# Kernel tuning notes

Hardware: AMD Instinct MI355X
Metric: run time of the kernel (lower is better)

Reference implementation:

```python
import jax, jax.numpy as jnp
import numpy as np

RESO = 32
SPLIT = 4
HEADS = 16  # block-level heads; each branch uses HEADS//2
DIM = 512
MLP_HID = 2048
EPS = 1e-5


def layer_norm(x, g, b):
    m = jnp.mean(x, axis=-1, keepdims=True)
    v = jnp.mean(jnp.square(x - m), axis=-1, keepdims=True)
    return (x - m) * jax.lax.rsqrt(v + EPS) * g + b


def dwconv3x3(x, w, b):
    # x: [N, C, Hs, Ws], w: [C, 1, 3, 3] (torch depthwise layout), b: [C]
    y = jax.lax.conv_general_dilated(
        x, w, window_strides=(1, 1), padding='SAME',
        feature_group_count=x.shape[1],
        dimension_numbers=('NCHW', 'OIHW', 'NCHW'))
    return y + b[None, :, None, None]


def cswin_branch(q, k, v, reso, Hs, Ws, heads, lepe_w, lepe_b):
    # q,k,v: [B, L, C] with L = reso^3; attention windows are Hs*Ws tokens,
    # window batch = B * D * (H/Hs) * (W/Ws) (depth folded into batch).
    B, L, C = q.shape
    hd = C // heads
    D = H = W = reso
    scale = hd ** -0.5

    def to_win(t):  # [B,L,C] -> [Bw, heads, Hs*Ws, hd]
        t = t.transpose(0, 2, 1).reshape(B, C, D, H // Hs, Hs, W // Ws, Ws)
        t = t.transpose(0, 2, 3, 5, 4, 6, 1).reshape(-1, Hs * Ws, heads, hd)
        return t.transpose(0, 2, 1, 3)

    qh = to_win(q)
    kh = to_win(k)
    # v windows kept in [Bw, C, Hs, Ws] image layout for the LePE depthwise conv
    vw = v.transpose(0, 2, 1).reshape(B, C, D, H // Hs, Hs, W // Ws, Ws)
    vw = vw.transpose(0, 2, 3, 5, 1, 4, 6).reshape(-1, C, Hs, Ws)
    lepe = dwconv3x3(vw, lepe_w, lepe_b)
    lepe = lepe.reshape(-1, heads, hd, Hs * Ws).transpose(0, 1, 3, 2)
    vh = vw.reshape(-1, heads, hd, Hs * Ws).transpose(0, 1, 3, 2)

    attn = jax.nn.softmax((qh * scale) @ jnp.swapaxes(kh, -1, -2), axis=-1)
    o = attn @ vh + lepe  # [Bw, heads, Hs*Ws, hd]

    # windows2img back to [B, L, C]
    o = o.transpose(0, 2, 1, 3).reshape(-1, Hs * Ws, C)
    o = o.reshape(B, D, H // Hs, W // Ws, Hs, Ws, C)
    o = o.transpose(0, 1, 2, 4, 3, 5, 6).reshape(B, D * H * W, C)
    return o


def setup_inputs() -> dict:
    key = jax.random.key(0)
    ks = jax.random.split(key, 16)
    C, Cb, hid = DIM, DIM // 2, MLP_HID

    def lin(k, fan_in, shape):
        return (jax.random.normal(k, shape, jnp.float32) * (fan_in ** -0.5))

    return {
        'x': jax.random.normal(ks[0], (1, C, RESO, RESO, RESO), jnp.float32),
        'norm1_g': jnp.ones((C,), jnp.float32),
        'norm1_b': jnp.zeros((C,), jnp.float32),
        'qkv_w': lin(ks[1], C, (C, 3 * C)),
        'lepe0_w': lin(ks[2], 9, (Cb, 1, 3, 3)),
        'lepe0_b': jnp.zeros((Cb,), jnp.float32),
        'lepe1_w': lin(ks[3], 9, (Cb, 1, 3, 3)),
        'lepe1_b': jnp.zeros((Cb,), jnp.float32),
        'proj_w': lin(ks[4], C, (C, C)),
        'proj_b': jnp.zeros((C,), jnp.float32),
        'norm2_g': jnp.ones((C,), jnp.float32),
        'norm2_b': jnp.zeros((C,), jnp.float32),
        'fc1_w': lin(ks[5], C, (C, hid)),
        'fc1_b': jnp.zeros((hid,), jnp.float32),
        'fc2_w': lin(ks[6], hid, (hid, C)),
        'fc2_b': jnp.zeros((C,), jnp.float32),
    }


def reference(x, norm1_g, norm1_b, qkv_w, lepe0_w, lepe0_b, lepe1_w, lepe1_b,
              proj_w, proj_b, norm2_g, norm2_b, fc1_w, fc1_b, fc2_w, fc2_b):
    B, C = x.shape[0], x.shape[1]
    reso = x.shape[2]
    xc = jnp.transpose(x, (0, 2, 3, 4, 1))  # [B,D,H,W,C]
    img = layer_norm(xc, norm1_g, norm1_b)
    qkv = jnp.einsum('bdhwc,co->bdhwo', img, qkv_w).reshape(B, -1, 3, C)
    q, k, v = qkv[:, :, 0], qkv[:, :, 1], qkv[:, :, 2]

    Ch = C // 2
    hh = HEADS // 2
    # branch 0: idx=0 -> H_sp=reso, W_sp=split ; branch 1: idx=1 -> H_sp=split, W_sp=reso
    x1 = cswin_branch(q[..., :Ch], k[..., :Ch], v[..., :Ch], reso, reso, SPLIT, hh, lepe0_w, lepe0_b)
    x2 = cswin_branch(q[..., Ch:], k[..., Ch:], v[..., Ch:], reso, SPLIT, reso, hh, lepe1_w, lepe1_b)
    att = jnp.concatenate([x1, x2], axis=2) @ proj_w + proj_b

    xf = xc.reshape(B, -1, C) + att
    h = layer_norm(xf, norm2_g, norm2_b)
    h = jax.nn.gelu(h @ fc1_w + fc1_b, approximate=False) @ fc2_w + fc2_b
    xf = xf + h
    out = xf.reshape(B, reso, reso, reso, C).transpose(0, 4, 1, 2, 3)
    return out
```

## Files before the change

### kernel.cpp

```cpp
#include <hip/hip_runtime.h>
#include <hip/hip_bf16.h>
#include <stdint.h>

typedef uint16_t u16;
typedef __attribute__((ext_vector_type(8))) short short8;
typedef __attribute__((ext_vector_type(4))) float floatx4;

#define MFMA(a, b, c) __builtin_amdgcn_mfma_f32_16x16x32_bf16((a), (b), (c), 0, 0, 0)
#define AS1(p) ((const __attribute__((address_space(1))) void*)(p))
#define AS3(p) ((__attribute__((address_space(3))) void*)(p))

static __device__ __forceinline__ float u2f(u16 u) {
    return __uint_as_float(((uint32_t)u) << 16);
}
static __device__ __forceinline__ u16 f2u(float f) {
    union { __hip_bfloat16 h; u16 u; } cv;
    cv.h = __float2bfloat16(f);
    return cv.u;
}
static __device__ __forceinline__ float ldf(const void* p, size_t i, bool f32m) {
    return f32m ? ((const float*)p)[i] : u2f(((const u16*)p)[i]);
}
static __device__ __forceinline__ short8 ld8(const void* p, size_t i, bool f32m) {
    if (f32m) {
        const float* f = (const float*)p + i;
        short8 o;
#pragma unroll
        for (int j = 0; j < 8; ++j) o[j] = (short)f2u(f[j]);
        return o;
    }
    return *reinterpret_cast<const short8*>((const u16*)p + i);
}
static __device__ __forceinline__ void st8(void* p, size_t i, const float* v, bool f32m) {
    if (f32m) {
        float* f = (float*)p + i;
#pragma unroll
        for (int j = 0; j < 8; ++j) f[j] = v[j];
    } else {
        short8 o;
#pragma unroll
        for (int j = 0; j < 8; ++j) o[j] = (short)f2u(v[j]);
        *reinterpret_cast<short8*>((u16*)p + i) = o;
    }
}
static __device__ __forceinline__ float gelu_f(float u) {
    float y = 1.5957691216057308f * (u + 0.044715f * u * u * u);
    return u / (1.f + __expf(-y));
}
static __device__ __forceinline__ void pl32swap(uint32_t& a, uint32_t& b) {
    asm volatile("v_permlane32_swap_b32 %0, %1" : "+v"(a), "+v"(b));
}

__global__ __launch_bounds__(256) void detect_dtype(const u16* __restrict__ x,
                                                    int* __restrict__ flag)
{
    const int tid = threadIdx.x;
    int cnt = 0;
    for (int i = tid; i < 4096; i += 256) {
        int e = (x[i] >> 7) & 0xFF;
        if (e >= 0xBE) ++cnt;
    }
#pragma unroll
    for (int m = 32; m >= 1; m >>= 1) cnt += __shfl_xor(cnt, m);
    __shared__ int s[4];
    if ((tid & 63) == 0) s[tid >> 6] = cnt;
    __syncthreads();
    if (tid == 0) flag[0] = (s[0] + s[1] + s[2] + s[3] >= 64) ? 1 : 0;
}

template <int MODE>
__global__ __launch_bounds__(256) void transpose_k(
    const void* __restrict__ src, void* __restrict__ dst, long dstOff,
    int R, int Cc, int dstS,
    const u16* __restrict__ add,
    const int* __restrict__ dflag, int srcSel, int dstSel)
{
    const bool iF = dflag[0] != 0;
    const bool sF = srcSel && iF;
    const bool dF = dstSel && iF;
    __shared__ __align__(16) u16 tile[64][72];
    const int tid = threadIdx.x;
    const int r0 = blockIdx.y * 64;
    const int c0 = blockIdx.x * 64;
#pragma unroll
    for (int s = 0; s < 2; ++s) {
        int ch = tid + s * 256;
        int ir = ch >> 3, ic = (ch & 7) * 8;
        short8 v = ld8(src, (size_t)(r0 + ir) * Cc + c0 + ic, sF);
        if constexpr (MODE == 3) {
            short8 a = *reinterpret_cast<const short8*>(add + (size_t)(r0 + ir) * Cc + c0 + ic);
#pragma unroll
            for (int j = 0; j < 8; ++j)
                tile[ir][ic + j] = f2u(u2f((u16)v[j]) + u2f((u16)a[j]));
        } else {
#pragma unroll
            for (int j = 0; j < 8; ++j) tile[ir][ic + j] = (u16)v[j];
        }
    }
    __syncthreads();
#pragma unroll
    for (int s = 0; s < 2; ++s) {
        int ch = tid + s * 256;
        int jr = ch >> 3, jc = (ch & 7) * 8;
        float f[8];
#pragma unroll
        for (int j = 0; j < 8; ++j) f[j] = u2f(tile[jc + j][jr]);
        st8(dst, (size_t)dstOff + (size_t)(c0 + jr) * dstS + r0 + jc, f, dF);
    }
}

__global__ __launch_bounds__(256) void tln64(
    const void* __restrict__ x, const void* __restrict__ g, const void* __restrict__ b,
    u16* __restrict__ O, u16* __restrict__ XT, const int* __restrict__ dflag)
{
    const bool iF = dflag[0] != 0;
    __shared__ __align__(16) u16 tile[64][520];
    const int tid = threadIdx.x;
    const int lane = tid & 63, w = tid >> 6;
    const int t0 = blockIdx.x * 64;
    for (int ct = 0; ct < 8; ++ct) {
#pragma unroll
        for (int s = 0; s < 2; ++s) {
            const int ch = tid + s * 256;
            const int ir = ch >> 3;
            const int ic = (ch & 7) * 8;
            const int c = ct * 64 + ir;
            short8 v = ld8(x, (size_t)c * 32768 + t0 + ic, iF);
            const int c8 = c >> 3;
            const int cl = c & 7;
#pragma unroll
            for (int j = 0; j < 8; ++j) {
                const int t = ic + j;
                const int pg = c8 ^ ((t >> 3) & 3);
                tile[t][pg * 8 + cl] = (u16)v[j];
            }
        }
    }
    __syncthreads();
    float gv[8], bv[8];
#pragma unroll
    for (int jj = 0; jj < 8; ++jj) {
        gv[jj] = ldf(g, lane * 8 + jj, iF);
        bv[jj] = ldf(b, lane * 8 + jj, iF);
    }
    for (int tt = 0; tt < 16; ++tt) {
        const int t = w * 16 + tt;
        const int pg = lane ^ ((t >> 3) & 3);
        short8 v = *reinterpret_cast<const short8*>(&tile[t][pg * 8]);
        *reinterpret_cast<short8*>(XT + (size_t)(t0 + t) * 512 + lane * 8) = v;
        float f[8];
        float s = 0.f, sq = 0.f;
#pragma unroll
        for (int jj = 0; jj < 8; ++jj) { f[jj] = u2f((u16)v[jj]); s += f[jj]; sq += f[jj] * f[jj]; }
#pragma unroll
        for (int m = 32; m >= 1; m >>= 1) { s += __shfl_xor(s, m); sq += __shfl_xor(sq, m); }
        const float mean = s * (1.f / 512.f);
        const float var = sq * (1.f / 512.f) - mean * mean;
        const float rstd = rsqrtf(var + 1e-5f);
        short8 o;
#pragma unroll
        for (int jj = 0; jj < 8; ++jj)
            o[jj] = (short)f2u((f[jj] - mean) * rstd * gv[jj] + bv[jj]);
        *reinterpret_cast<short8*>(O + (size_t)(t0 + t) * 512 + lane * 8) = o;
    }
}

__global__ __launch_bounds__(256) void ln512(
    const u16* __restrict__ X, const void* __restrict__ g, const void* __restrict__ b,
    u16* __restrict__ O, const int* __restrict__ dflag)
{
    const bool iF = dflag[0] != 0;
    const int wid = threadIdx.x >> 6, lane = threadIdx.x & 63;
    const int row = blockIdx.x * 4 + wid;
    const size_t base = (size_t)row * 512 + lane * 8;
    short8 v = *reinterpret_cast<const short8*>(X + base);
    float f[8];
    float s = 0.f, sq = 0.f;
#pragma unroll
    for (int j = 0; j < 8; ++j) { f[j] = u2f((u16)v[j]); s += f[j]; sq += f[j] * f[j]; }
#pragma unroll
    for (int m = 32; m >= 1; m >>= 1) { s += __shfl_xor(s, m); sq += __shfl_xor(sq, m); }
    const float mean = s * (1.f / 512.f);
    const float var = sq * (1.f / 512.f) - mean * mean;
    const float rstd = rsqrtf(var + 1e-5f);
    short8 o;
#pragma unroll
    for (int j = 0; j < 8; ++j)
        o[j] = (short)f2u((f[j] - mean) * rstd * ldf(g, lane * 8 + j, iF)
                          + ldf(b, lane * 8 + j, iF));
    *reinterpret_cast<short8*>(O + base) = o;
}

template <int EPI>
__global__ __launch_bounds__(256) void gemm_bt(
    const u16* __restrict__ A, const u16* __restrict__ Bt,
    const void* __restrict__ bias,
    u16* __restrict__ Cout, int Nt, int N, int K, const int* __restrict__ dflag)
{
    const bool iF = dflag[0] != 0;
    __shared__ __align__(16) u16 As[2][128 * 32];
    __shared__ __align__(16) u16 Bs[2][128 * 32];
    const int bidf = blockIdx.x;
    const int xcd = bidf & 7;
    const int j = bidf >> 3;
    const int m_blk = (j / Nt) * 8 + xcd;
    const int n_blk = j % Nt;
    const int tid = threadIdx.x;
    const int lane = tid & 63, wid = tid >> 6;
    const int wm = wid >> 1, wn = wid & 1;
    const int quad = lane >> 4, l15 = lane & 15;

    floatx4 zero4 = {0.f, 0.f, 0.f, 0.f};
    floatx4 acc[4][4];
#pragma unroll
    for (int i = 0; i < 4; ++i)
#pragma unroll
        for (int jj = 0; jj < 4; ++jj) acc[i][jj] = zero4;

    const u16* Ab = A + (size_t)m_blk * 128 * K;
    const u16* Bb = Bt + (size_t)n_blk * 128 * K;
    const int r0 = tid >> 2;
    const int k0o = (tid & 3) * 8;

    for (int kk = 0; kk < K; kk += 64) {
        if (kk) __syncthreads();
#pragma unroll
        for (int h = 0; h < 2; ++h) {
            const int kg = kk + h * 32 + k0o;
            char* dA = (char*)As[h] + wid * 1024;
            char* dB = (char*)Bs[h] + wid * 1024;
            __builtin_amdgcn_global_load_lds(AS1(Ab + (size_t)r0 * K + kg),        AS3(dA), 16, 0, 0);
            __builtin_amdgcn_global_load_lds(AS1(Ab + (size_t)(r0 + 64) * K + kg), AS3(dA + 4096), 16, 0, 0);
            __builtin_amdgcn_global_load_lds(AS1(Bb + (size_t)r0 * K + kg),        AS3(dB), 16, 0, 0);
            __builtin_amdgcn_global_load_lds(AS1(Bb + (size_t)(r0 + 64) * K + kg), AS3(dB + 4096), 16, 0, 0);
        }
        __syncthreads();
#pragma unroll
        for (int h = 0; h < 2; ++h) {
            short8 af[4], bfv[4];
#pragma unroll
            for (int i = 0; i < 4; ++i)
                af[i] = *reinterpret_cast<const short8*>(&As[h][(wm * 64 + i * 16 + l15) * 32 + quad * 8]);
#pragma unroll
            for (int jj = 0; jj < 4; ++jj)
                bfv[jj] = *reinterpret_cast<const short8*>(&Bs[h][(wn * 64 + jj * 16 + l15) * 32 + quad * 8]);
#pragma unroll
            for (int i = 0; i < 4; ++i)
#pragma unroll
                for (int jj = 0; jj < 4; ++jj)
                    acc[i][jj] = MFMA(af[i], bfv[jj], acc[i][jj]);
        }
    }

    const int m_base = m_blk * 128 + wm * 64 + quad * 4;
    const int n_base = n_blk * 128 + wn * 64 + l15;
#pragma unroll
    for (int i = 0; i < 4; ++i) {
#pragma unroll
        for (int jj = 0; jj < 4; ++jj) {
            const int n = n_base + jj * 16;
            float badd = 0.f;
            if constexpr (EPI >= 1) badd = ldf(bias, n, iF);
#pragma unroll
            for (int r = 0; r < 4; ++r) {
                const int m = m_base + i * 16 + r;
                float v = acc[i][jj][r] + badd;
                if constexpr (EPI == 3) v = gelu_f(v);
                Cout[(size_t)m * N + n] = f2u(v);
            }
        }
    }
}

#define STG(slot, mat, kh, Gb, kcol) do {                                        \
    char* _d = (char*)&L[(slot)][(mat)][(kh)][0] + ldsofs;                       \
    __builtin_amdgcn_global_load_lds(AS1((Gb) + (size_t)srow0 * K + (kcol) + scol0),         AS3(_d),        16, 0, 0); \
    __builtin_amdgcn_global_load_lds(AS1((Gb) + (size_t)(srow0 + 128) * K + (kcol) + scol0), AS3(_d + 8192), 16, 0, 0); \
} while (0)

#define VMW(n) do { asm volatile("s_waitcnt vmcnt(" #n ")" ::: "memory");        \
                    __builtin_amdgcn_sched_barrier(0); } while (0)

#define PHASE(s, kh, nq, STAGE_STMT, WAIT_STMT) do {                             \
    const char* Au = (const char*)&L[(s)][0][(kh)][0];                           \
    const char* Bu = (const char*)&L[(s)][1][(kh)][0];                           \
    if ((nq) == 0) {                                                             \
        _Pragma("unroll")                                                        \
        for (int mf = 0; mf < 8; ++mf)                                           \
            af[mf] = *reinterpret_cast<const short8*>(Au + aoff[mf]);            \
    }                                                                            \
    short8 b0 = *reinterpret_cast<const short8*>(Bu + boff[nq][0]);              \
    short8 b1 = *reinterpret_cast<const short8*>(Bu + boff[nq][1]);              \
    STAGE_STMT;                                                                  \
    asm volatile("s_barrier" ::: "memory");                                      \
    asm volatile("s_waitcnt lgkmcnt(0)" ::: "memory");                           \
    __builtin_amdgcn_sched_barrier(0);                                           \
    __builtin_amdgcn_s_setprio(1);                                               \
    _Pragma("unroll")                                                            \
    for (int mf = 0; mf < 8; ++mf) {                                             \
        acc[mf][(nq) * 2]     = MFMA(af[mf], b0, acc[mf][(nq) * 2]);             \
        acc[mf][(nq) * 2 + 1] = MFMA(af[mf], b1, acc[mf][(nq) * 2 + 1]);         \
    }                                                                            \
    __builtin_amdgcn_s_setprio(0);                                               \
    WAIT_STMT;                                                                   \
    asm volatile("s_barrier" ::: "memory");                                      \
} while (0)

#define GROUP(g, W2, W4, S12, S34) do {                                          \
    const int _s = (g) & 1;                                                      \
    PHASE(_s, 0, 0, if (S12) STG(_s ^ 1, 0, 1, Ab, ((g) + 1) * 64 + 32), (void)0); \
    PHASE(_s, 0, 1, if (S12) STG(_s ^ 1, 1, 1, Bb, ((g) + 1) * 64 + 32), W2);    \
    PHASE(_s, 1, 0, if (S34) STG(_s,     0, 0, Ab, ((g) + 2) * 64),      (void)0); \
    PHASE(_s, 1, 1, if (S34) STG(_s,     1, 0, Bb, ((g) + 2) * 64),      W4);    \
} while (0)

template <int EPI>
__global__ __launch_bounds__(512, 2) void gemm256_bt(
    const u16* __restrict__ A, const u16* __restrict__ Bt,
    const void* __restrict__ bias,
    u16* __restrict__ Cout, int Nt, int N, int K,
    const u16* __restrict__ xadd,
    const int* __restrict__ dflag)
{
    const bool iF = dflag[0] != 0;
    __shared__ __align__(16) u16 L[2][2][2][8192];
    const int bidf = blockIdx.x;
    const int xcd = bidf & 7;
    const int j = bidf >> 3;
    const int m_blk = (j / Nt) * 8 + xcd;
    const int n_blk = j % Nt;
    const int tid = threadIdx.x;
    const int lane = tid & 63, wid = tid >> 6;
    const int wm = wid >> 2, wn = wid & 3;
    const int quad = lane >> 4, l15 = lane & 15;

    const int srow0 = wid * 16 + (lane >> 2);
    const int scol0 = ((lane & 3) ^ ((srow0 >> 1) & 3)) * 8;
    const int ldsofs = wid * 1024;

    const u16* Ab = A + (size_t)m_blk * 256 * K;
    const u16* Bb = Bt + (size_t)n_blk * 256 * K;

    const int sq = (quad ^ ((l15 >> 1) & 3)) << 4;
    int aoff[8], boff[2][2];
#pragma unroll
    for (int mf = 0; mf < 8; ++mf)
        aoff[mf] = (wm * 128 + mf * 16 + l15) * 64 + sq;
#pragma unroll
    for (int nq = 0; nq < 2; ++nq)
#pragma unroll
        for (int jj = 0; jj < 2; ++jj)
            boff[nq][jj] = (wn * 64 + nq * 32 + jj * 16 + l15) * 64 + sq;

    floatx4 zero4 = {0.f, 0.f, 0.f, 0.f};
    floatx4 acc[8][4];
#pragma unroll
    for (int i = 0; i < 8; ++i)
#pragma unroll
        for (int jj = 0; jj < 4; ++jj) acc[i][jj] = zero4;
    short8 af[8];

    const int NG = K >> 6;

    STG(0, 0, 0, Ab, 0);
    STG(0, 1, 0, Bb, 0);
    STG(0, 0, 1, Ab, 32);
    STG(0, 1, 1, Bb, 32);
    STG(1, 0, 0, Ab, 64);
    STG(1, 1, 0, Bb, 64);
    VMW(8);
    asm volatile("s_barrier" ::: "memory");

    int g = 0;
    for (; g < NG - 2; ++g) GROUP(g, VMW(8), VMW(8), true, true);
    GROUP(g, VMW(8), VMW(4), true, false); ++g;
    GROUP(g, VMW(0), (void)0, false, false);

    const int m0 = m_blk * 256 + wm * 128 + quad * 4;
    const int n0 = n_blk * 256 + wn * 64 + l15;
#pragma unroll
    for (int mf = 0; mf < 8; ++mf) {
#pragma unroll
        for (int nf = 0; nf < 4; ++nf) {
            const int n = n0 + nf * 16;
            float badd = 0.f;
            if constexpr (EPI >= 1) badd = ldf(bias, n, iF);
#pragma unroll
            for (int r = 0; r < 4; ++r) {
                const int m = m0 + mf * 16 + r;
                float v = acc[mf][nf][r] + badd;
                if constexpr (EPI == 2) v += u2f(xadd[(size_t)m * 512 + n]);
                if constexpr (EPI == 3) v = gelu_f(v);
                Cout[(size_t)m * N + n] = f2u(v);
            }
        }
    }
}

__global__ __launch_bounds__(256) void cswin_attn(
    const u16* __restrict__ qkv,
    const void* __restrict__ lepe0_w, const void* __restrict__ lepe0_b,
    const void* __restrict__ lepe1_w, const void* __restrict__ lepe1_b,
    u16* __restrict__ att, const int* __restrict__ dflag)
{
    const bool iF = dflag[0] != 0;
    __shared__ __align__(16) u16 q_s[4096];
    __shared__ __align__(16) u16 k_s[4096];
    __shared__ __align__(16) u16 vt_s[32 * 130];
    __shared__ float lw_s[32 * 9];
    __shared__ float lb_s[32];

    const int bid = blockIdx.x;
    const int branch = bid >> 11;
    const int rr = bid & 2047;
    const int win = rr >> 3, head = rr & 7;
    const int d = win >> 3, blk = win & 7;
    const int tid = threadIdx.x;
    const int lane = tid & 63, wid = tid >> 6;
    const int quad = lane >> 4, l15 = lane & 15;
    const int choff = branch * 256 + head * 32;
    const int dbase = d * 1024;

    const void* lw = branch ? lepe1_w : lepe0_w;
    const void* lbp = branch ? lepe1_b : lepe0_b;
    for (int i = tid; i < 288; i += 256) lw_s[i] = ldf(lw, head * 288 + i, iF);
    if (tid < 32) lb_s[tid] = ldf(lbp, head * 32 + tid, iF);

#pragma unroll
    for (int s = 0; s < 2; ++s) {
        int ch = tid + s * 256;
        int t = ch >> 2, e0 = (ch & 3) * 8;
        int l = branch ? (dbase + blk * 128 + t)
                       : (dbase + (t >> 2) * 32 + blk * 4 + (t & 3));
        size_t rowo = (size_t)l * 1536 + choff + e0;
        short8 qv = *reinterpret_cast<const short8*>(qkv + rowo);
        short8 kv = *reinterpret_cast<const short8*>(qkv + rowo + 512);
        short8 vv = *reinterpret_cast<const short8*>(qkv + rowo + 1024);
        const int sw = ((ch >> 3) & 3) << 3;
        *reinterpret_cast<short8*>(&q_s[(ch * 8) ^ sw]) = qv;
        *reinterpret_cast<short8*>(&k_s[(ch * 8) ^ sw]) = kv;
#pragma unroll
        for (int j = 0; j < 8; ++j) vt_s[(e0 + j) * 130 + t] = (u16)vv[j];
    }
    __syncthreads();

    floatx4 zero4 = {0.f, 0.f, 0.f, 0.f};
    const int sq8 = (quad ^ ((l15 >> 1) & 3)) * 8;
    short8 qf[2];
#pragma unroll
    for (int qi = 0; qi < 2; ++qi)
        qf[qi] = *reinterpret_cast<const short8*>(&q_s[(wid * 32 + qi * 16 + l15) * 32 + sq8]);
    floatx4 st[8][2];
#pragma unroll
    for (int kt = 0; kt < 8; ++kt) { st[kt][0] = zero4; st[kt][1] = zero4; }
#pragma unroll
    for (int kt = 0; kt < 8; ++kt) {
        short8 kf = *reinterpret_cast<const short8*>(&k_s[(kt * 16 + l15) * 32 + sq8]);
        st[kt][0] = MFMA(kf, qf[0], st[kt][0]);
        st[kt][1] = MFMA(kf, qf[1], st[kt][1]);
    }

    const float scale = 0.17677669529663687f;
    float inv[2];
#pragma unroll
    for (int qi = 0; qi < 2; ++qi) {
        float sum = 0.f;
#pragma unroll
        for (int kt = 0; kt < 8; ++kt)
#pragma unroll
            for (int r = 0; r < 4; ++r) {
                float v = __expf(st[kt][qi][r] * scale);
                st[kt][qi][r] = v;
                sum += v;
            }
        sum += __shfl_xor(sum, 16);
        sum += __shfl_xor(sum, 32);
        inv[qi] = 1.f / sum;
    }
    uint32_t pk[2][8][2];
#pragma unroll
    for (int qi = 0; qi < 2; ++qi)
#pragma unroll
        for (int kt = 0; kt < 8; ++kt)
#pragma unroll
            for (int u = 0; u < 2; ++u)
                pk[qi][kt][u] = (uint32_t)f2u(st[kt][qi][2 * u] * inv[qi])
                              | ((uint32_t)f2u(st[kt][qi][2 * u + 1] * inv[qi]) << 16);
#pragma unroll
    for (int qi = 0; qi < 2; ++qi)
#pragma unroll
        for (int t = 0; t < 4; ++t)
#pragma unroll
            for (int u = 0; u < 2; ++u)
                pl32swap(pk[qi][2 * t][u], pk[qi][2 * t + 1][u]);

    const uint32_t* v32 = (const uint32_t*)vt_s;
    const int hi4 = (lane >> 4) & 1;
    floatx4 oacc[2][2];
#pragma unroll
    for (int qi = 0; qi < 2; ++qi) { oacc[qi][0] = zero4; oacc[qi][1] = zero4; }
#pragma unroll
    for (int ks = 0; ks < 4; ++ks) {
        const int kq = ks * 16 + quad * 4;
        union { uint32_t w[4]; short8 s; } bv[2];
#pragma unroll
        for (int j = 0; j < 2; ++j) {
            const int chan = j * 16 + l15;
#pragma unroll
            for (int q = 0; q < 4; ++q) bv[j].w[q] = v32[chan * 65 + kq + q];
        }
#pragma unroll
        for (int qi = 0; qi < 2; ++qi) {
            const uint32_t a0 = pk[qi][2 * ks][0],     a1 = pk[qi][2 * ks][1];
            const uint32_t b0 = pk[qi][2 * ks + 1][0], b1 = pk[qi][2 * ks + 1][1];
            const uint32_t s0 = (uint32_t)__shfl_xor((int)a0, 16);
            const uint32_t s1 = (uint32_t)__shfl_xor((int)a1, 16);
            const uint32_t t0 = (uint32_t)__shfl_xor((int)b0, 16);
            const uint32_t t1 = (uint32_t)__shfl_xor((int)b1, 16);
            union { uint32_t w[4]; short8 s; } gw;
            gw.w[0] = hi4 ? t0 : a0;
            gw.w[1] = hi4 ? t1 : a1;
            gw.w[2] = hi4 ? b0 : s0;
            gw.w[3] = hi4 ? b1 : s1;
            oacc[qi][0] = MFMA(gw.s, bv[0].s, oacc[qi][0]);
            oacc[qi][1] = MFMA(gw.s, bv[1].s, oacc[qi][1]);
        }
    }

    const int Hs = branch ? 4 : 32;
    const int Wsz = branch ? 32 : 4;
    const int wsl = branch ? 5 : 2;
    const int wmask = Wsz - 1;
#pragma unroll
    for (int ii = 0; ii < 2; ++ii) {
        const int t0 = wid * 32 + ii * 16 + quad * 4;
        const int hi0 = t0 >> wsl;
        const int w0 = t0 & wmask;
        const int y0 = (hi0 > 0) ? -1 : 0;
        const int y1 = (hi0 < Hs - 1) ? 1 : 0;
        const bool xm = (w0 > 0);
        const bool xp = (w0 + 4 < Wsz);
#pragma unroll
        for (int j = 0; j < 2; ++j) {
            const int e = j * 16 + l15;
            float val[4];
#pragma unroll
            for (int r = 0; r < 4; ++r) val[r] = oacc[ii][j][r] + lb_s[e];
            const uint32_t* vrow = v32 + e * 65;
            const float* wrow = &lw_s[e * 9];
            for (int dy = y0; dy <= y1; ++dy) {
                const int rowb = (hi0 + dy) << wsl;
                const int wlo = rowb >> 1;
                const int whi = wlo + (Wsz >> 1) - 1;
                const int wb = wlo + (w0 >> 1);
                int c0 = wb - 1; if (c0 < wlo) c0 = wlo;
                int c3 = wb + 2; if (c3 > whi) c3 = whi;
                const uint32_t u0 = vrow[c0];
                const uint32_t u1 = vrow[wb];
                const uint32_t u2 = vrow[wb + 1];
                const uint32_t u3 = vrow[c3];
                const float em1 = __uint_as_float(u0 & 0xffff0000u);
                const float f0 = __uint_as_float(u1 << 16);
                const float f1 = __uint_as_float(u1 & 0xffff0000u);
                const float f2 = __uint_as_float(u2 << 16);
                const float f3 = __uint_as_float(u2 & 0xffff0000u);
                const float f4 = __uint_as_float(u3 << 16);
                const float* w3 = wrow + (dy + 1) * 3;
                const float wl = w3[0], wc = w3[1], wp = w3[2];
                const float wl0 = xm ? wl : 0.f;
                const float wp3 = xp ? wp : 0.f;
                val[0] += wl0 * em1 + wc * f0 + wp * f1;
                val[1] += wl * f0 + wc * f1 + wp * f2;
                val[2] += wl * f1 + wc * f2 + wp * f3;
                val[3] += wl * f2 + wc * f3 + wp3 * f4;
            }
#pragma unroll
            for (int r = 0; r < 4; ++r) {
                const int t = t0 + r;
                const int l = branch ? (dbase + blk * 128 + t)
                                     : (dbase + (t >> 2) * 32 + blk * 4 + (t & 3));
                att[(size_t)l * 512 + choff + e] = f2u(val[r]);
            }
        }
    }
}

extern "C" void kernel_launch(void* const* d_in, const int* in_sizes, int n_in,
                              void* d_out, int out_size, void* d_ws, size_t ws_size,
                              hipStream_t stream)
{
    const void* x      = d_in[0];
    const void* n1g    = d_in[1];
    const void* n1b    = d_in[2];
    const void* qkv_w  = d_in[3];
    const void* l0w    = d_in[4];
    const void* l0b    = d_in[5];
    const void* l1w    = d_in[6];
    const void* l1b    = d_in[7];
    const void* proj_w = d_in[8];
    const void* proj_b = d_in[9];
    const void* n2g    = d_in[10];
    const void* n2b    = d_in[11];
    const void* fc1_w  = d_in[12];
    const void* fc1_b  = d_in[13];
    const void* fc2_w  = d_in[14];
    const void* fc2_b  = d_in[15];

    const size_t MB = 1ull << 20;
    if (ws_size < 104 * MB) return;

    char* w = (char*)d_ws;
    u16* qkvT  = (u16*)(w + 0 * MB);
    u16* projT = (u16*)(w + 2 * MB);
    u16* fc1T  = (u16*)(w + 3 * MB);
    u16* fc2T  = (u16*)(w + 5 * MB);
    int* flag  = (int*)(w + 7 * MB);
    u16* qkvb  = (u16*)(w + 8 * MB);
    u16* xf    = (u16*)(w + 40 * MB);
    u16* ln2oc = (u16*)(w + 8 * MB);
    u16* yf    = (u16*)(w + 72 * MB);
    u16* img   = (u16*)d_out;
    u16* xT    = (u16*)d_out + 16777216;
    u16* attb  = (u16*)d_out;
    u16* h1c   = (u16*)d_out;

    const dim3 B(256);
    const dim3 B512(512);
    const u16* NUL = nullptr;
    const void* NULV = nullptr;

    detect_dtype<<<dim3(1), B, 0, stream>>>((const u16*)x, flag);

    transpose_k<0><<<dim3(24, 8), B, 0, stream>>>(qkv_w, qkvT, 0, 512, 1536, 512, NUL, flag, 1, 0);
    transpose_k<0><<<dim3(8, 8),  B, 0, stream>>>(proj_w, projT, 0, 512, 512, 512, NUL, flag, 1, 0);
    transpose_k<0><<<dim3(32, 8), B, 0, stream>>>(fc1_w, fc1T, 0, 512, 2048, 512, NUL, flag, 1, 0);
    transpose_k<0><<<dim3(8, 32), B, 0, stream>>>(fc2_w, fc2T, 0, 2048, 512, 2048, NUL, flag, 1, 0);

    tln64<<<dim3(512), B, 0, stream>>>(x, n1g, n1b, img, xT, flag);

    gemm256_bt<0><<<dim3(128 * 6), B512, 0, stream>>>(img, qkvT, NULV, qkvb, 6, 1536, 512, NUL, flag);

    cswin_attn<<<dim3(4096), B, 0, stream>>>(qkvb, l0w, l0b, l1w, l1b, attb, flag);

    gemm256_bt<2><<<dim3(128 * 2), B512, 0, stream>>>(attb, projT, proj_b, xf, 2, 512, 512, xT, flag);

    for (int i = 0; i < 2; ++i) {
        const size_t off = (size_t)i * 16384 * 512;
        ln512<<<dim3(4096), B, 0, stream>>>(xf + off, n2g, n2b, ln2oc, flag);
        gemm256_bt<3><<<dim3(64 * 8), B512, 0, stream>>>(ln2oc, fc1T, fc1_b, h1c, 8, 2048, 512, NUL, flag);
        gemm_bt<1><<<dim3(128 * 4), B, 0, stream>>>(h1c, fc2T, fc2_b, yf + off, 4, 512, 2048, flag);
    }
    transpose_k<3><<<dim3(8, 512), B, 0, stream>>>(yf, d_out, 0, 32768, 512, 32768, xf, flag, 0, 1);
}
```

Before: 603.9 us.

## Fold LayerNorm2 into fc1 GEMM epilogue and fuse residual transpose into fc2

Replaces the per-chunk LayerNorm kernel with a single row-stats pass and folds the norm algebraically into the fc1 GEMM: gamma is pre-multiplied into the transposed fc1 weights, and the epilogue applies mean/rstd plus the precomputed column sums of gamma*W and beta*W. The fc2 GEMM epilogue now adds the residual and writes directly in transposed NCDHW layout, removing the final transpose kernel and the yf buffer. The fc1 output is split across two workspace buffers. The aim is to remove a full read/write pass of the normalized activations and the final transpose, at the cost of uncoalesced 4-element transposed stores and some precision change from the folded norm.

Measured after the change: 633.0 us. 1.05x slower.

```diff
diff --git a/kernel.cpp b/kernel.cpp
--- a/kernel.cpp
+++ b/kernel.cpp
@@ -87,15 +87,8 @@
         int ch = tid + s * 256;
         int ir = ch >> 3, ic = (ch & 7) * 8;
         short8 v = ld8(src, (size_t)(r0 + ir) * Cc + c0 + ic, sF);
-        if constexpr (MODE == 3) {
-            short8 a = *reinterpret_cast<const short8*>(add + (size_t)(r0 + ir) * Cc + c0 + ic);
-#pragma unroll
-            for (int j = 0; j < 8; ++j)
-                tile[ir][ic + j] = f2u(u2f((u16)v[j]) + u2f((u16)a[j]));
-        } else {
-#pragma unroll
-            for (int j = 0; j < 8; ++j) tile[ir][ic + j] = (u16)v[j];
-        }
+#pragma unroll
+        for (int j = 0; j < 8; ++j) tile[ir][ic + j] = (u16)v[j];
     }
     __syncthreads();
 #pragma unroll
@@ -165,37 +158,61 @@
     }
 }
 
-__global__ __launch_bounds__(256) void ln512(
-    const u16* __restrict__ X, const void* __restrict__ g, const void* __restrict__ b,
-    u16* __restrict__ O, const int* __restrict__ dflag)
-{
-    const bool iF = dflag[0] != 0;
+__global__ __launch_bounds__(256) void ln_stats(
+    const u16* __restrict__ X, float* __restrict__ S)
+{
     const int wid = threadIdx.x >> 6, lane = threadIdx.x & 63;
     const int row = blockIdx.x * 4 + wid;
     const size_t base = (size_t)row * 512 + lane * 8;
     short8 v = *reinterpret_cast<const short8*>(X + base);
-    float f[8];
     float s = 0.f, sq = 0.f;
 #pragma unroll
-    for (int j = 0; j < 8; ++j) { f[j] = u2f((u16)v[j]); s += f[j]; sq += f[j] * f[j]; }
+    for (int j = 0; j < 8; ++j) { float f = u2f((u16)v[j]); s += f; sq += f * f; }
 #pragma unroll
     for (int m = 32; m >= 1; m >>= 1) { s += __shfl_xor(s, m); sq += __shfl_xor(sq, m); }
-    const float mean = s * (1.f / 512.f);
-    const float var = sq * (1.f / 512.f) - mean * mean;
-    const float rstd = rsqrtf(var + 1e-5f);
-    short8 o;
-#pragma unroll
-    for (int j = 0; j < 8; ++j)
-        o[j] = (short)f2u((f[j] - mean) * rstd * ldf(g, lane * 8 + j, iF)
-                          + ldf(b, lane * 8 + j, iF));
-    *reinterpret_cast<short8*>(O + base) = o;
+    if (lane == 0) {
+        const float mean = s * (1.f / 512.f);
+        const float var = sq * (1.f / 512.f) - mean * mean;
+        float2 st; st.x = mean; st.y = rsqrtf(var + 1e-5f);
+        reinterpret_cast<float2*>(S)[row] = st;
+    }
+}
+
+__global__ __launch_bounds__(256) void colvec(
+    const void* __restrict__ W, const void* __restrict__ g, const void* __restrict__ b,
+    float* __restrict__ gw, float* __restrict__ bw, const int* __restrict__ dflag)
+{
+    const bool iF = dflag[0] != 0;
+    const int n = blockIdx.x * 256 + threadIdx.x;
+    float sg = 0.f, sb = 0.f;
+    for (int k = 0; k < 512; ++k) {
+        const float wv = ldf(W, (size_t)k * 2048 + n, iF);
+        sg += ldf(g, k, iF) * wv;
+        sb += ldf(b, k, iF) * wv;
+    }
+    gw[n] = sg;
+    bw[n] = sb;
+}
+
+__global__ __launch_bounds__(256) void scalek(
+    u16* __restrict__ T, const void* __restrict__ g, const int* __restrict__ dflag)
+{
+    const bool iF = dflag[0] != 0;
+    const size_t i = ((size_t)blockIdx.x * 256 + threadIdx.x) * 8;
+    short8 v = *reinterpret_cast<const short8*>(T + i);
+    const int k0 = (int)(i & 511);
+#pragma unroll
+    for (int j = 0; j < 8; ++j) v[j] = (short)f2u(u2f((u16)v[j]) * ldf(g, k0 + j, iF));
+    *reinterpret_cast<short8*>(T + i) = v;
 }
 
 template <int EPI>
 __global__ __launch_bounds__(256) void gemm_bt(
-    const u16* __restrict__ A, const u16* __restrict__ Bt,
-    const void* __restrict__ bias,
-    u16* __restrict__ Cout, int Nt, int N, int K, const int* __restrict__ dflag)
+    const u16* __restrict__ A, const u16* __restrict__ A2, int aSplit,
+    const u16* __restrict__ Bt, const void* __restrict__ bias,
+    u16* __restrict__ Cout, int Nt, int N, int K,
+    const u16* __restrict__ xadd, void* __restrict__ outp, int tokOff,
+    const int* __restrict__ dflag)
 {
     const bool iF = dflag[0] != 0;
     __shared__ __align__(16) u16 As[2][128 * 32];
@@ -217,7 +234,9 @@
 #pragma unroll
         for (int jj = 0; jj < 4; ++jj) acc[i][jj] = zero4;
 
-    const u16* Ab = A + (size_t)m_blk * 128 * K;
+    const u16* Ab = (A2 && m_blk >= aSplit)
+                  ? A2 + (size_t)(m_blk - aSplit) * 128 * K
+                  : A + (size_t)m_blk * 128 * K;
     const u16* Bb = Bt + (size_t)n_blk * 128 * K;
     const int r0 = tid >> 2;
     const int k0o = (tid & 3) * 8;
@@ -261,12 +280,31 @@
             const int n = n_base + jj * 16;
             float badd = 0.f;
             if constexpr (EPI >= 1) badd = ldf(bias, n, iF);
-#pragma unroll
-            for (int r = 0; r < 4; ++r) {
-                const int m = m_base + i * 16 + r;
-                float v = acc[i][jj][r] + badd;
-                if constexpr (EPI == 3) v = gelu_f(v);
-                Cout[(size_t)m * N + n] = f2u(v);
+            if constexpr (EPI == 4) {
+                float vv[4];
+#pragma unroll
+                for (int r = 0; r < 4; ++r) {
+                    const int m = m_base + i * 16 + r;
+                    vv[r] = acc[i][jj][r] + badd + u2f(xadd[(size_t)m * 512 + n]);
+                }
+                const size_t ob = (size_t)n * 32768 + tokOff + m_base + i * 16;
+                if (iF) {
+                    floatx4 v4 = {vv[0], vv[1], vv[2], vv[3]};
+                    *reinterpret_cast<floatx4*>((float*)outp + ob) = v4;
+                } else {
+                    union { u16 a[4]; uint2 v; } pk;
+#pragma unroll
+                    for (int r = 0; r < 4; ++r) pk.a[r] = f2u(vv[r]);
+                    *reinterpret_cast<uint2*>((u16*)outp + ob) = pk.v;
+                }
+            } else {
+#pragma unroll
+                for (int r = 0; r < 4; ++r) {
+                    const int m = m_base + i * 16 + r;
+                    float v = acc[i][jj][r] + badd;
+                    if constexpr (EPI == 3) v = gelu_f(v);
+                    Cout[(size_t)m * N + n] = f2u(v);
+                }
             }
         }
     }
@@ -318,8 +356,11 @@
 __global__ __launch_bounds__(512, 2) void gemm256_bt(
     const u16* __restrict__ A, const u16* __restrict__ Bt,
     const void* __restrict__ bias,
-    u16* __restrict__ Cout, int Nt, int N, int K,
+    u16* __restrict__ Cout, u16* __restrict__ Cout2, int mSplit,
+    int Nt, int N, int K,
     const u16* __restrict__ xadd,
+    const float* __restrict__ s2, const float* __restrict__ gwv,
+    const float* __restrict__ bwv,
     const int* __restrict__ dflag)
 {
     const bool iF = dflag[0] != 0;
@@ -376,22 +417,41 @@
     GROUP(g, VMW(8), VMW(4), true, false); ++g;
     GROUP(g, VMW(0), (void)0, false, false);
 
+    u16* Co = Cout;
+    int mOff = 0;
+    if (EPI == 5 && Cout2 && m_blk >= mSplit) { Co = Cout2; mOff = mSplit * 256; }
+
     const int m0 = m_blk * 256 + wm * 128 + quad * 4;
     const int n0 = n_blk * 256 + wn * 64 + l15;
 #pragma unroll
     for (int mf = 0; mf < 8; ++mf) {
+        float mn[4], rs[4];
+        if constexpr (EPI == 5) {
+#pragma unroll
+            for (int r = 0; r < 4; ++r) {
+                const float2 st = reinterpret_cast<const float2*>(s2)[m0 + mf * 16 + r];
+                mn[r] = st.x; rs[r] = st.y;
+            }
+        }
 #pragma unroll
         for (int nf = 0; nf < 4; ++nf) {
             const int n = n0 + nf * 16;
             float badd = 0.f;
             if constexpr (EPI >= 1) badd = ldf(bias, n, iF);
+            float gwn = 0.f, bwn = 0.f;
+            if constexpr (EPI == 5) { gwn = gwv[n]; bwn = bwv[n]; }
 #pragma unroll
             for (int r = 0; r < 4; ++r) {
                 const int m = m0 + mf * 16 + r;
-                float v = acc[mf][nf][r] + badd;
-                if constexpr (EPI == 2) v += u2f(xadd[(size_t)m * 512 + n]);
-                if constexpr (EPI == 3) v = gelu_f(v);
-                Cout[(size_t)m * N + n] = f2u(v);
+                float v;
+                if constexpr (EPI == 5) {
+                    v = rs[r] * (acc[mf][nf][r] - mn[r] * gwn) + bwn + badd;
+                    v = gelu_f(v);
+                } else {
+                    v = acc[mf][nf][r] + badd;
+                    if constexpr (EPI == 2) v += u2f(xadd[(size_t)m * 512 + n]);
+                }
+                Co[(size_t)(m - mOff) * N + n] = f2u(v);
             }
         }
     }
@@ -615,19 +675,23 @@
     u16* fc1T  = (u16*)(w + 3 * MB);
     u16* fc2T  = (u16*)(w + 5 * MB);
     int* flag  = (int*)(w + 7 * MB);
+    float* gw  = (float*)(w + 7 * MB + 4096);
+    float* bw  = (float*)(w + 7 * MB + 16384);
+    float* stats = (float*)(w + 7 * MB + 32768);
     u16* qkvb  = (u16*)(w + 8 * MB);
+    u16* h1cA  = (u16*)(w + 8 * MB);
     u16* xf    = (u16*)(w + 40 * MB);
-    u16* ln2oc = (u16*)(w + 8 * MB);
-    u16* yf    = (u16*)(w + 72 * MB);
+    u16* h1cB  = (u16*)(w + 72 * MB);
     u16* img   = (u16*)d_out;
     u16* xT    = (u16*)d_out + 16777216;
     u16* attb  = (u16*)d_out;
-    u16* h1c   = (u16*)d_out;
 
     const dim3 B(256);
     const dim3 B512(512);
     const u16* NUL = nullptr;
+    u16* NULN = nullptr;
     const void* NULV = nullptr;
+    const float* NULF = nullptr;
 
     detect_dtype<<<dim3(1), B, 0, stream>>>((const u16*)x, flag);
 
@@ -635,20 +699,26 @@
     transpose_k<0><<<dim3(8, 8),  B, 0, stream>>>(proj_w, projT, 0, 512, 512, 512, NUL, flag, 1, 0);
     transpose_k<0><<<dim3(32, 8), B, 0, stream>>>(fc1_w, fc1T, 0, 512, 2048, 512, NUL, flag, 1, 0);
     transpose_k<0><<<dim3(8, 32), B, 0, stream>>>(fc2_w, fc2T, 0, 2048, 512, 2048, NUL, flag, 1, 0);
+    scalek<<<dim3(512), B, 0, stream>>>(fc1T, n2g, flag);
+    colvec<<<dim3(8), B, 0, stream>>>(fc1_w, n2g, n2b, gw, bw, flag);
 
     tln64<<<dim3(512), B, 0, stream>>>(x, n1g, n1b, img, xT, flag);
 
-    gemm256_bt<0><<<dim3(128 * 6), B512, 0, stream>>>(img, qkvT, NULV, qkvb, 6, 1536, 512, NUL, flag);
+    gemm256_bt<0><<<dim3(128 * 6), B512, 0, stream>>>(img, qkvT, NULV, qkvb, NULN, 0, 6, 1536, 512, NUL, NULF, NULF, NULF, flag);
 
     cswin_attn<<<dim3(4096), B, 0, stream>>>(qkvb, l0w, l0b, l1w, l1b, attb, flag);
 
-    gemm256_bt<2><<<dim3(128 * 2), B512, 0, stream>>>(attb, projT, proj_b, xf, 2, 512, 512, xT, flag);
+    gemm256_bt<2><<<dim3(128 * 2), B512, 0, stream>>>(attb, projT, proj_b, xf, NULN, 0, 2, 512, 512, xT, NULF, NULF, NULF, flag);
+
+    ln_stats<<<dim3(8192), B, 0, stream>>>(xf, stats);
 
     for (int i = 0; i < 2; ++i) {
-        const size_t off = (size_t)i * 16384 * 512;
-        ln512<<<dim3(4096), B, 0, stream>>>(xf + off, n2g, n2b, ln2oc, flag);
-        gemm256_bt<3><<<dim3(64 * 8), B512, 0, stream>>>(ln2oc, fc1T, fc1_b, h1c, 8, 2048, 512, NUL, flag);
-        gemm_bt<1><<<dim3(128 * 4), B, 0, stream>>>(h1c, fc2T, fc2_b, yf + off, 4, 512, 2048, flag);
-    }
-    transpose_k<3><<<dim3(8, 512), B, 0, stream>>>(yf, d_out, 0, 32768, 512, 32768, xf, flag, 0, 1);
-}
+        const int tok0 = i * 16384;
+        const size_t off = (size_t)tok0 * 512;
+        gemm256_bt<5><<<dim3(64 * 8), B512, 0, stream>>>(xf + off, fc1T, fc1_b,
+            h1cA, h1cB, 32, 8, 2048, 512, NUL,
+            stats + (size_t)tok0 * 2, gw, bw, flag);
+        gemm_bt<4><<<dim3(128 * 4), B, 0, stream>>>(h1cA, h1cB, 64, fc2T, fc2_b,
+            NULN, 4, 512, 2048, xf + off, d_out, tok0, flag);
+    }
+}
```
